# Kernel optimization log

Measured on AMD Instinct MI355X. Metric: run time of the kernel, lower is better.

The kernel has to match this reference:

```python
import jax, jax.numpy as jnp
import numpy as np

HEADS = 4
NBLK = 4
UPS = 4
EPS = 1e-5


def conv3x3(x, w, b):
    # x: NCHW, w: OIHW (3x3, stride 1, pad 1 -> SAME)
    y = jax.lax.conv_general_dilated(x, w, (1, 1), 'SAME',
                                     dimension_numbers=('NCHW', 'OIHW', 'NCHW'))
    return y + b[None, :, None, None]


def layer_norm(x, g, b):
    mu = jnp.mean(x, axis=-1, keepdims=True)
    var = jnp.var(x, axis=-1, keepdims=True)
    return (x - mu) * jax.lax.rsqrt(var + EPS) * g + b


def attention(x, wq, bq, wp, bp):
    # NOTE: the torch module's reshape flattens all windows into one sequence,
    # so this is mathematically global attention over all H*W tokens.
    B, H, W, C = x.shape
    L = H * W
    hd = C // HEADS
    t = x.reshape(B, L, C)
    qkv = (t @ wq + bq).reshape(B, L, 3, HEADS, hd).transpose(2, 0, 3, 1, 4)
    q, k, v = qkv[0], qkv[1], qkv[2]                      # (B, nh, L, hd)
    attn = jax.nn.softmax(jnp.einsum('bnld,bnmd->bnlm', q, k) * (hd ** -0.5), axis=-1)
    o = jnp.einsum('bnlm,bnmd->bnld', attn, v)            # (B, nh, L, hd)
    o = o.transpose(0, 2, 1, 3).reshape(B, L, C)
    return (o @ wp + bp).reshape(B, H, W, C)


def swin_block(x, g1, b1, wq, bq, wp, bp, g2, b2, w1, bf1, w2, bf2):
    shortcut = x
    h = jnp.transpose(x, (0, 2, 3, 1))                    # NHWC
    h = layer_norm(h, g1, b1)
    h = attention(h, wq, bq, wp, bp) + h
    h = layer_norm(h, g2, b2)
    h = (jax.nn.gelu(h @ w1 + bf1, approximate=False) @ w2 + bf2) + h
    return shortcut + jnp.transpose(h, (0, 3, 1, 2))


def pixel_shuffle(x, r):
    B, C, H, W = x.shape
    c = C // (r * r)
    x = x.reshape(B, c, r, r, H, W).transpose(0, 1, 4, 2, 5, 3)
    return x.reshape(B, c, H * r, W * r)


def setup_inputs() -> dict:
    key = jax.random.key(0)
    ks = jax.random.split(key, 16)
    d = 48

    def rn(k, shape, s=0.02):
        return jax.random.normal(k, shape, jnp.float32) * s

    return {
        'x': jax.random.normal(ks[0], (2, 3, 64, 64), jnp.float32),
        'conv_first_w': rn(ks[1], (d, 3, 3, 3)),
        'conv_first_b': jnp.zeros((d,), jnp.float32),
        'norm1_g': jnp.ones((NBLK, d), jnp.float32),
        'norm1_b': jnp.zeros((NBLK, d), jnp.float32),
        'qkv_w': rn(ks[2], (NBLK, d, 3 * d)),
        'qkv_b': jnp.zeros((NBLK, 3 * d), jnp.float32),
        'proj_w': rn(ks[3], (NBLK, d, d)),
        'proj_b': jnp.zeros((NBLK, d), jnp.float32),
        'norm2_g': jnp.ones((NBLK, d), jnp.float32),
        'norm2_b': jnp.zeros((NBLK, d), jnp.float32),
        'fc1_w': rn(ks[4], (NBLK, d, 2 * d)),
        'fc1_b': jnp.zeros((NBLK, 2 * d), jnp.float32),
        'fc2_w': rn(ks[5], (NBLK, 2 * d, d)),
        'fc2_b': jnp.zeros((NBLK, d), jnp.float32),
        'up_w': rn(ks[6], (d * UPS * UPS, d, 3, 3)),
        'up_b': jnp.zeros((d * UPS * UPS,), jnp.float32),
        'last_w': rn(ks[7], (3, d, 3, 3)),
        'last_b': jnp.zeros((3,), jnp.float32),
    }


def reference(x, conv_first_w, conv_first_b, norm1_g, norm1_b, qkv_w, qkv_b,
              proj_w, proj_b, norm2_g, norm2_b, fc1_w, fc1_b, fc2_w, fc2_b,
              up_w, up_b, last_w, last_b):
    h = conv3x3(x, conv_first_w, conv_first_b)
    for i in range(NBLK):
        h = swin_block(h, norm1_g[i], norm1_b[i], qkv_w[i], qkv_b[i],
                       proj_w[i], proj_b[i], norm2_g[i], norm2_b[i],
                       fc1_w[i], fc1_b[i], fc2_w[i], fc2_b[i])
    h = conv3x3(h, up_w, up_b)
    h = pixel_shuffle(h, UPS)
    return conv3x3(h, last_w, last_b)
```

## Files before the change

kernel.cpp:

```cpp
#include <hip/hip_runtime.h>
#include <hip/hip_bf16.h>
#include <math.h>

#define BB 2
#define D 48
#define HH 64
#define WW 64
#define LL 4096
#define NHEADS 4
#define HD 12
#define NBLK 4
#define CUP 768
#define H2 256
#define W2 256

#define NSPLIT 4
#define OPART_STRIDE 393216

typedef __attribute__((ext_vector_type(8))) short short8v;
typedef __attribute__((ext_vector_type(4))) float f32x4;
typedef unsigned long long u64;

__device__ __forceinline__ short f2bf(float f) {
    __hip_bfloat16 h = __float2bfloat16(f);
    union { __hip_bfloat16 b; short s; } u; u.b = h; return u.s;
}
__device__ __forceinline__ float bf2f(short s) {
    union { float f; unsigned u; } x;
    x.u = ((unsigned)(unsigned short)s) << 16;
    return x.f;
}
__device__ __forceinline__ float exp2_raw(float x) {
    float r; asm("v_exp_f32 %0, %1" : "=v"(r) : "v"(x)); return r;
}

__global__ void conv3x3_kernel(const float* __restrict__ in, const float* __restrict__ w,
                               const float* __restrict__ bias, float* __restrict__ out,
                               int Cin, int Cout) {
    int idx = blockIdx.x * blockDim.x + threadIdx.x;
    int total = BB * Cout * HH * WW;
    if (idx >= total) return;
    int x = idx % WW;
    int y = (idx / WW) % HH;
    int co = (idx / (WW * HH)) % Cout;
    int b = idx / (WW * HH * Cout);
    float s = bias[co];
    for (int ci = 0; ci < Cin; ci++) {
        const float* ip = in + ((size_t)(b * Cin + ci) * HH) * WW;
        const float* wp = w + (size_t)(co * Cin + ci) * 9;
        #pragma unroll
        for (int ky = 0; ky < 3; ky++) {
            int iy = y + ky - 1;
            if (iy < 0 || iy >= HH) continue;
            #pragma unroll
            for (int kx = 0; kx < 3; kx++) {
                int ix = x + kx - 1;
                if (ix < 0 || ix >= WW) continue;
                s += ip[iy * WW + ix] * wp[ky * 3 + kx];
            }
        }
    }
    out[idx] = s;
}

__global__ __launch_bounds__(256) void pack_h_kernel(const float* __restrict__ h,
                                                     short* __restrict__ hbfp) {
    int idx = blockIdx.x * 256 + threadIdx.x;
    const int TOT = 2 * 66 * 66 * 48;
    if (idx >= TOT + 64) return;
    if (idx >= TOT) { hbfp[idx] = 0; return; }
    int ci = idx % 48;
    int p = idx / 48;
    int xx = p % 66;
    int q = p / 66;
    int yy = q % 66;
    int b = q / 66;
    short v = 0;
    if (yy >= 1 && yy <= 64 && xx >= 1 && xx <= 64)
        v = f2bf(h[((size_t)(b * 48 + ci) << 12) + (yy - 1) * 64 + (xx - 1)]);
    hbfp[idx] = v;
}

__global__ __launch_bounds__(256) void pack_w_kernel(const float* __restrict__ w,
                                                     short* __restrict__ Wp) {
    int idx = blockIdx.x * 256 + threadIdx.x;
    if (idx >= 48 * 14 * 512) return;
    int j = idx & 7;
    int g = (idx >> 3) & 3;
    int col = (idx >> 5) & 15;
    int s = (idx >> 9) % 14;
    int n16 = idx / (14 * 512);
    int k = 32 * s + 8 * g + j;
    short v = 0;
    if (k < 432) {
        int tap = k / 48, ci = k - tap * 48;
        int co = n16 * 16 + col;
        v = f2bf(w[((size_t)co * 48 + ci) * 9 + tap]);
    }
    Wp[idx] = v;
}

__global__ __launch_bounds__(256) void pack_lw_kernel(const float* __restrict__ w,
                                                      short* __restrict__ Wp2) {
    int idx = blockIdx.x * 256 + threadIdx.x;
    if (idx >= 14 * 512) return;
    int j = idx & 7;
    int g = (idx >> 3) & 3;
    int col = (idx >> 5) & 15;
    int s = idx >> 9;
    int k = 32 * s + 8 * g + j;
    short v = 0;
    if (k < 432 && col < 3) {
        int tap = k / 48, ci = k - tap * 48;
        v = f2bf(w[((size_t)col * 48 + ci) * 9 + tap]);
    }
    Wp2[idx] = v;
}

#define CU_LOADB(P, n) { \
    _Pragma("unroll") \
    for (int s_ = 0; s_ < 14; s_++) \
        P[s_] = *(const short8v*)(Wb + (size_t)(n) * 7168 + s_ * 512); }

#define CU_COMP(P, n) { \
    f32x4 acc = {0.f, 0.f, 0.f, 0.f}; \
    _Pragma("unroll") \
    for (int s_ = 0; s_ < 14; s_++) \
        acc = __builtin_amdgcn_mfma_f32_16x16x32_bf16(av[s_], P[s_], acc, 0, 0, 0); \
    float bval = bias[(n) * 16 + col]; \
    _Pragma("unroll") \
    for (int j = 0; j < 4; j++) \
        Sw[sbase + j * 192 + (n)] = f2bf(acc[j] + bval); }

__global__ __launch_bounds__(128) void conv_up_mfma_kernel(const short* __restrict__ hbfp,
                                                           const short* __restrict__ Wp,
                                                           const float* __restrict__ bias,
                                                           short* __restrict__ U) {
    __shared__ short Sb[2][12288];
    int tid = threadIdx.x;
    int wave = tid >> 6, lane = tid & 63;
    int mt = blockIdx.x * 2 + wave;
    int b = mt >> 8;
    int rem = mt & 255;
    int y = rem >> 2;
    int xt = rem & 3;
    int col = lane & 15;
    int g = lane >> 4;
    int x = xt * 16 + col;

    const short* zb = hbfp + 2 * 66 * 66 * 48;

    short8v av[14];
    #pragma unroll
    for (int s = 0; s < 14; s++) {
        int gg = 4 * s + g;
        int tap = (gg * 171) >> 10;
        int cig = gg - tap * 6;
        int dy = (tap * 11) >> 5;
        int dx = tap - dy * 3;
        const short* ap = hbfp + ((size_t)((b * 66 + y + dy) * 66 + (x + dx)) * 48 + cig * 8);
        ap = (gg < 54) ? ap : zb;
        av[s] = *(const short8v*)ap;
    }

    const short* Wb = Wp + col * 32 + g * 8;
    short* Sw = Sb[wave];
    int dyq = col >> 2, dxq = col & 3;
    int sbase = dyq * 3072 + (16 * g + dxq) * 48;

    short8v Ba[14], Bb[14];
    CU_LOADB(Ba, 0);
    for (int n = 0; n < 48; n += 2) {
        CU_LOADB(Bb, n + 1);
        CU_COMP(Ba, n);
        if (n + 2 < 48) CU_LOADB(Ba, n + 2);
        CU_COMP(Bb, n + 1);
    }

    short* Ub = U + (((size_t)(b * 256 + 4 * y) * 256) + xt * 64) * 48;
    for (int i = lane; i < 1536; i += 64) {
        int row = i / 384;
        int w8 = i - row * 384;
        short8v v = *(const short8v*)(Sw + (size_t)i * 8);
        *(short8v*)(Ub + (size_t)row * 256 * 48 + w8 * 8) = v;
    }
}

__global__ void zero16_kernel(u64* __restrict__ p, int n) {
    int i = blockIdx.x * 256 + threadIdx.x;
    if (i >= n) return;
    u64 fill = 0ull;
    int rel = 8 * i - 2097152;
    if (rel >= 0 && rel < 524288 && (((rel >> 5) & 15) == 12))
        fill = 0x3F803F803F803F80ull;
    p[2 * i] = fill;
    p[2 * i + 1] = fill;
}

__global__ __launch_bounds__(256) void fused_ln1_qkv_kernel(
    const float* __restrict__ hsrc, const float* __restrict__ g1, const float* __restrict__ b1,
    const float* __restrict__ w, const float* __restrict__ bias,
    float* __restrict__ ln1, short* __restrict__ Qbf, short* __restrict__ Kbf,
    short* __restrict__ Vr) {
    __shared__ float hs[48 * 17];
    __shared__ float lnr[16 * 49];
    __shared__ float wl[48 * 144];
    int blk = blockIdx.x;
    int b = blk >> 8;
    int pos0 = (blk & 255) * 16;
    int tid = threadIdx.x;

    for (int i = tid; i < 48 * 144; i += 256) wl[i] = w[i];
    for (int i = tid; i < 48 * 16; i += 256) {
        int ch = i >> 4, p = i & 15;
        hs[ch * 17 + p] = hsrc[((size_t)b * 48 + ch) * 4096 + pos0 + p];
    }
    __syncthreads();

    int tok = tid >> 4, oct = tid & 15;
    int pos = pos0 + tok;
    float v[3];
    float s = 0.f, s2 = 0.f;
    #pragma unroll
    for (int j = 0; j < 3; j++) {
        float x = hs[(oct * 3 + j) * 17 + tok];
        v[j] = x; s += x; s2 += x * x;
    }
    #pragma unroll
    for (int msk = 1; msk < 16; msk <<= 1) {
        s += __shfl_xor(s, msk, 64);
        s2 += __shfl_xor(s2, msk, 64);
    }
    float mu = s * (1.f / 48.f);
    float var = s2 * (1.f / 48.f) - mu * mu;
    float rs = rsqrtf(var + 1e-5f);
    float* go = ln1 + ((size_t)b * 4096 + pos) * 48 + oct * 3;
    #pragma unroll
    for (int j = 0; j < 3; j++) {
        int c = oct * 3 + j;
        float y = (v[j] - mu) * rs * g1[c] + b1[c];
        lnr[tok * 49 + c] = y;
        go[j] = y;
    }
    __syncthreads();

    int c0 = oct * 9;
    float acc[9];
    #pragma unroll
    for (int j = 0; j < 9; j++) acc[j] = bias[c0 + j];
    #pragma unroll 4
    for (int k = 0; k < 48; k++) {
        float a = lnr[tok * 49 + k];
        const float* wr = wl + k * 144 + c0;
        #pragma unroll
        for (int j = 0; j < 9; j++) acc[j] += a * wr[j];
    }

    const float scale = 0.41647023f;
    int sstep = pos >> 5, r = pos & 31;
    int g2 = (r < 16) ? (r >> 2) : ((r - 16) >> 2);
    int j2 = (r < 16) ? (r & 3) : 4 + ((r - 16) & 3);
    #pragma unroll
    for (int j = 0; j < 9; j++) {
        int c = c0 + j;
        int which = (c >= 96) ? 2 : (c >= 48 ? 1 : 0);
        int rem = c - which * 48;
        int hh = rem / 12;
        int dd = rem - hh * 12;
        int bh = b * 4 + hh;
        if (which == 0)
            Qbf[((size_t)bh * 4096 + pos) * 32 + dd] = f2bf(acc[j] * scale);
        else if (which == 1)
            Kbf[((size_t)bh * 4096 + pos) * 32 + dd] = f2bf(acc[j]);
        else
            Vr[((size_t)bh * 128 + sstep) * 512 + dd * 32 + g2 * 8 + j2] = f2bf(acc[j]);
    }
}

__global__ __launch_bounds__(256) void fused_mlp_kernel(
    const float* __restrict__ opart, const float* __restrict__ ssump,
    const float* __restrict__ pwg, const float* __restrict__ pb,
    const float* __restrict__ ln1, const float* __restrict__ g2v, const float* __restrict__ b2v,
    const float* __restrict__ f1w, const float* __restrict__ f1b,
    const float* __restrict__ f2w, const float* __restrict__ f2b,
    float* __restrict__ hbuf) {
    __shared__ float sm[14640];
    float* wp  = sm;
    float* w1  = sm + 2304;
    float* w2  = sm + 6912;
    float* arf = sm + 11520;
    float* lnr = sm + 12304;
    float* m1v = sm + 13088;

    int blk = blockIdx.x;
    int b = blk >> 8;
    int pos0 = (blk & 255) * 16;
    int tid = threadIdx.x;

    for (int i = tid; i < 2304; i += 256) wp[i] = pwg[i];
    for (int i = tid; i < 4608; i += 256) w1[i] = f1w[i];
    for (int i = tid; i < 4608; i += 256) w2[i] = f2w[i];
    for (int i = tid; i < 768; i += 256) {
        int t = i / 48, c = i - (i / 48) * 48;
        int hh = c / 12;
        size_t base = ((size_t)b * 4096 + pos0) * 48 + i;
        float stot = 0.f, s = 0.f;
        #pragma unroll
        for (int sp = 0; sp < NSPLIT; sp++) {
            stot += ssump[((size_t)sp * 8 + b * 4 + hh) * 4096 + pos0 + t];
            s += opart[base + (size_t)sp * OPART_STRIDE];
        }
        arf[t * 49 + c] = s / stot;
    }
    __syncthreads();

    int tok = tid >> 4, oct = tid & 15;
    size_t gtok = (size_t)b * 4096 + pos0 + tok;
    int c0 = oct * 3;
    float acc[3];
    #pragma unroll
    for (int j = 0; j < 3; j++) acc[j] = pb[c0 + j];
    #pragma unroll 4
    for (int k = 0; k < 48; k++) {
        float a = arf[tok * 49 + k];
        const float* wr = wp + k * 48 + c0;
        #pragma unroll
        for (int j = 0; j < 3; j++) acc[j] += a * wr[j];
    }
    const float* rp = ln1 + gtok * 48 + c0;
    float x[3]; float s = 0.f, s2 = 0.f;
    #pragma unroll
    for (int j = 0; j < 3; j++) {
        float t = acc[j] + rp[j];
        x[j] = t; s += t; s2 += t * t;
    }
    #pragma unroll
    for (int msk = 1; msk < 16; msk <<= 1) {
        s += __shfl_xor(s, msk, 64);
        s2 += __shfl_xor(s2, msk, 64);
    }
    float mu = s * (1.f / 48.f), var = s2 * (1.f / 48.f) - mu * mu;
    float rs = rsqrtf(var + 1e-5f);
    #pragma unroll
    for (int j = 0; j < 3; j++) {
        int c = c0 + j;
        lnr[tok * 49 + c] = (x[j] - mu) * rs * g2v[c] + b2v[c];
    }
    __syncthreads();

    int d0 = oct * 6;
    float a2[6];
    #pragma unroll
    for (int j = 0; j < 6; j++) a2[j] = f1b[d0 + j];
    #pragma unroll 4
    for (int k = 0; k < 48; k++) {
        float a = lnr[tok * 49 + k];
        const float* wr = w1 + k * 96 + d0;
        #pragma unroll
        for (int j = 0; j < 6; j++) a2[j] += a * wr[j];
    }
    #pragma unroll
    for (int j = 0; j < 6; j++) {
        float g = a2[j];
        m1v[tok * 97 + d0 + j] = 0.5f * g * (1.f + erff(g * 0.70710678118654752f));
    }
    __syncthreads();

    float f2acc[3];
    #pragma unroll
    for (int j = 0; j < 3; j++) f2acc[j] = f2b[c0 + j];
    #pragma unroll 4
    for (int k = 0; k < 96; k++) {
        float a = m1v[tok * 97 + k];
        const float* wr = w2 + k * 48 + c0;
        #pragma unroll
        for (int j = 0; j < 3; j++) f2acc[j] += a * wr[j];
    }
    __syncthreads();
    #pragma unroll
    for (int j = 0; j < 3; j++)
        arf[tok * 49 + c0 + j] = f2acc[j] + lnr[tok * 49 + c0 + j];
    __syncthreads();

    for (int i = tid; i < 768; i += 256) {
        int c = i >> 4, t = i & 15;
        hbuf[(((size_t)(b * 48 + c)) << 12) + pos0 + t] += arf[t * 49 + c];
    }
}

#define LOADCH(P, c) { \
    _Pragma("unroll") \
    for (int s_ = 0; s_ < 4; s_++) { \
        const short* kp_ = Kb + ((size_t)((c) * 128 + s_ * 32 + col)) * 32 + g * 8; \
        P##k0[s_] = *(const short8v*)(kp_); \
        P##k1[s_] = *(const short8v*)(kp_ + 512); \
        P##v[s_]  = *(const short8v*)(Vrb + ((c) * 4 + s_) * 512 + vbase); \
    } }

#define STEP4(kc0, kc1, vv) { \
    _Pragma("unroll") \
    for (int f_ = 0; f_ < 4; f_++) { \
        f32x4 z_ = {0.f, 0.f, 0.f, 0.f}; \
        f32x4 s1 = __builtin_amdgcn_mfma_f32_16x16x32_bf16(kc0, qb[f_], z_, 0, 0, 0); \
        f32x4 s2 = __builtin_amdgcn_mfma_f32_16x16x32_bf16(kc1, qb[f_], z_, 0, 0, 0); \
        float p0 = exp2_raw(s1[0]), p1 = exp2_raw(s1[1]); \
        float p2 = exp2_raw(s1[2]), p3 = exp2_raw(s1[3]); \
        float p4 = exp2_raw(s2[0]), p5 = exp2_raw(s2[1]); \
        float p6 = exp2_raw(s2[2]), p7 = exp2_raw(s2[3]); \
        union { short8v sv; unsigned u[4]; } pu_; \
        asm("v_cvt_pk_bf16_f32 %0, %1, %2" : "=v"(pu_.u[0]) : "v"(p0), "v"(p1)); \
        asm("v_cvt_pk_bf16_f32 %0, %1, %2" : "=v"(pu_.u[1]) : "v"(p2), "v"(p3)); \
        asm("v_cvt_pk_bf16_f32 %0, %1, %2" : "=v"(pu_.u[2]) : "v"(p4), "v"(p5)); \
        asm("v_cvt_pk_bf16_f32 %0, %1, %2" : "=v"(pu_.u[3]) : "v"(p6), "v"(p7)); \
        o[f_] = __builtin_amdgcn_mfma_f32_16x16x32_bf16(vv, pu_.sv, o[f_], 0, 0, 0); \
    } }

#define COMPUTECH4(P) { \
    STEP4(P##k0[0], P##k1[0], P##v[0]); \
    STEP4(P##k0[1], P##k1[1], P##v[1]); \
    STEP4(P##k0[2], P##k1[2], P##v[2]); \
    STEP4(P##k0[3], P##k1[3], P##v[3]); }

__global__ __launch_bounds__(256) void attn_mfma_kernel(const short* __restrict__ Qbf,
                                                        const short* __restrict__ Kbf,
                                                        const short* __restrict__ Vr,
                                                        float* __restrict__ opart,
                                                        float* __restrict__ ssump) {
    int bid = blockIdx.x;
    int bh = bid & 7;
    int qblk = (bid >> 3) & 15;
    int split = bid >> 7;
    int h = bh & 3, b = bh >> 2;
    int tid = threadIdx.x;
    int wave = tid >> 6;
    int lane = tid & 63;
    int q0 = qblk * 256 + wave * 64;
    int col = lane & 15;
    int g = lane >> 4;

    const short* Kb  = Kbf + (size_t)bh * LL * 32 + (size_t)split * 1024 * 32;
    const short* Vrb = Vr + (size_t)bh * 65536 + (size_t)split * 32 * 512;
    int vbase = col * 32 + g * 8;

    short8v qb[4];
    f32x4 o[4];
    #pragma unroll
    for (int f = 0; f < 4; f++) {
        qb[f] = *(const short8v*)(Qbf + ((size_t)bh * LL + q0 + 16 * f + col) * 32 + g * 8);
        o[f] = (f32x4){0.f, 0.f, 0.f, 0.f};
    }

    short8v a_k0[4], a_k1[4], a_v[4];
    short8v b_k0[4], b_k1[4], b_v[4];

    LOADCH(a_, 0);
    for (int c = 0; c < 8; c += 2) {
        LOADCH(b_, c + 1);
        COMPUTECH4(a_);
        if (c + 2 < 8) LOADCH(a_, c + 2);
        COMPUTECH4(b_);
    }

    #pragma unroll
    for (int f = 0; f < 4; f++) {
        float ss = __shfl(o[f][0], 48 + col, 64);
        float* op = opart + (size_t)split * OPART_STRIDE
                  + ((size_t)b * 4096 + q0 + 16 * f + col) * 48 + h * HD;
        #pragma unroll
        for (int j = 0; j < 4; j++) {
            int d = 4 * g + j;
            if (d < HD)
                op[d] = o[f][j];
        }
        if (lane < 16)
            ssump[((size_t)split * 8 + bh) * 4096 + q0 + 16 * f + col] = ss;
    }
}

__global__ __launch_bounds__(256) void lastconv_mfma_kernel(const short* __restrict__ U,
                                                            const short* __restrict__ Wp2,
                                                            const short* __restrict__ zb,
                                                            const float* __restrict__ bias,
                                                            float* __restrict__ out) {
    int tid = threadIdx.x;
    int wave = tid >> 6, lane = tid & 63;
    int t = blockIdx.x * 4 + wave;
    int xt = t & 15;
    int yy = (t >> 4) & 255;
    int b = t >> 12;
    int col = lane & 15, g = lane >> 4;
    int x = xt * 16 + col;

    const short* Ub = U + (size_t)b * 65536 * 48;
    const short* Bp = Wp2 + col * 32 + g * 8;

    f32x4 acc = {0.f, 0.f, 0.f, 0.f};
    #pragma unroll
    for (int s = 0; s < 14; s++) {
        int gg = 4 * s + g;
        int tap = (gg * 171) >> 10;
        int cig = gg - tap * 6;
        int dy3 = (tap * 11) >> 5;
        int dy = dy3 - 1;
        int dx = tap - dy3 * 3 - 1;
        int yq = yy + dy, xq = x + dx;
        bool ok = (gg < 54) && (yq >= 0) && (yq < 256) && (xq >= 0) && (xq < 256);
        const short* ap = Ub + (ptrdiff_t)(yq * 256 + xq) * 48 + cig * 8;
        ap = ok ? ap : zb;
        short8v av = *(const short8v*)ap;
        short8v bv = *(const short8v*)(Bp + s * 512);
        acc = __builtin_amdgcn_mfma_f32_16x16x32_bf16(av, bv, acc, 0, 0, 0);
    }

    if (col < 3) {
        float bval = bias[col];
        float* op = out + ((size_t)(b * 3 + col) * 256 + yy) * 256 + xt * 16 + 4 * g;
        #pragma unroll
        for (int j = 0; j < 4; j++)
            op[j] = acc[j] + bval;
    }
}

static inline int gs(int n) { return (n + 255) / 256; }

extern "C" void kernel_launch(void* const* d_in, const int* in_sizes, int n_in,
                              void* d_out, int out_size, void* d_ws, size_t ws_size,
                              hipStream_t stream) {
    const float* x    = (const float*)d_in[0];
    const float* cf_w = (const float*)d_in[1];
    const float* cf_b = (const float*)d_in[2];
    const float* n1g  = (const float*)d_in[3];
    const float* n1b  = (const float*)d_in[4];
    const float* qkvw = (const float*)d_in[5];
    const float* qkvb = (const float*)d_in[6];
    const float* pw   = (const float*)d_in[7];
    const float* pb   = (const float*)d_in[8];
    const float* n2g  = (const float*)d_in[9];
    const float* n2b  = (const float*)d_in[10];
    const float* f1w  = (const float*)d_in[11];
    const float* f1b  = (const float*)d_in[12];
    const float* f2w  = (const float*)d_in[13];
    const float* f2b  = (const float*)d_in[14];
    const float* upw  = (const float*)d_in[15];
    const float* upb  = (const float*)d_in[16];
    const float* lw   = (const float*)d_in[17];
    const float* lb   = (const float*)d_in[18];

    float* ws = (float*)d_ws;
    const int S_h = BB * D * LL;
    float* A_h   = ws;
    float* pool  = ws + S_h;
    float* A_ln1 = pool;

    short* U_bf = (short*)pool;
    float* o_part = pool + 1572864;
    short* Qbf  = (short*)(pool + 3538944);
    short* Kbf  = Qbf + BB * NHEADS * LL * 32;
    short* Vr   = Kbf + BB * NHEADS * LL * 32;
    short* hbfp = (short*)(pool + 4849664);
    short* Wp   = (short*)(pool + 5058784);
    short* Wp2  = (short*)(pool + 5230816);
    float* ssum_part = pool + 5898240;

    conv3x3_kernel<<<gs(S_h), 256, 0, stream>>>(x, cf_w, cf_b, A_h, 3, D);

    zero16_kernel<<<1536, 256, 0, stream>>>((u64*)Qbf, 393216);
    pack_w_kernel<<<1344, 256, 0, stream>>>(upw, Wp);
    pack_lw_kernel<<<28, 256, 0, stream>>>(lw, Wp2);

    for (int i = 0; i < NBLK; i++) {
        fused_ln1_qkv_kernel<<<512, 256, 0, stream>>>(
            A_h, n1g + i * D, n1b + i * D,
            qkvw + (size_t)i * D * 3 * D, qkvb + i * 3 * D,
            A_ln1, Qbf, Kbf, Vr);
        attn_mfma_kernel<<<8 * 16 * NSPLIT, 256, 0, stream>>>(Qbf, Kbf, Vr, o_part, ssum_part);
        fused_mlp_kernel<<<512, 256, 0, stream>>>(
            o_part, ssum_part, pw + (size_t)i * D * D, pb + i * D,
            A_ln1, n2g + i * D, n2b + i * D,
            f1w + (size_t)i * D * 2 * D, f1b + i * 2 * D,
            f2w + (size_t)i * 2 * D * D, f2b + i * D,
            A_h);
    }

    pack_h_kernel<<<1634, 256, 0, stream>>>(A_h, hbfp);
    conv_up_mfma_kernel<<<256, 128, 0, stream>>>(hbfp, Wp, upb, U_bf);

    lastconv_mfma_kernel<<<2048, 256, 0, stream>>>(
        U_bf, Wp2, hbfp + 2 * 66 * 66 * 48, lb, (float*)d_out);
}
```

Baseline: 278.9 us.

## Double attention key splits and split conv_up output channels across waves

The attention kernel now splits the key/value sequence into 8 chunks instead of 4, doubling the grid so each block processes half as many key chunks. The partial-output workspace is rearranged so the larger set of partial results fits. The upsampling conv kernel now uses 4 waves per block: two waves share each output tile, each computing half of the 48 output-channel groups, with a block-wide barrier before a cooperative store. This raises parallelism in both kernels, at the cost of more partial sums for the MLP kernel to merge and a synchronisation in conv_up.

Result: no change. 282.7 us (+1.4%).

```diff
diff --git a/kernel.cpp b/kernel.cpp
--- a/kernel.cpp
+++ b/kernel.cpp
@@ -14,7 +14,7 @@
 #define H2 256
 #define W2 256
 
-#define NSPLIT 4
+#define NSPLIT 8
 #define OPART_STRIDE 393216
 
 typedef __attribute__((ext_vector_type(8))) short short8v;
@@ -132,14 +132,16 @@
     for (int j = 0; j < 4; j++) \
         Sw[sbase + j * 192 + (n)] = f2bf(acc[j] + bval); }
 
-__global__ __launch_bounds__(128) void conv_up_mfma_kernel(const short* __restrict__ hbfp,
+__global__ __launch_bounds__(256) void conv_up_mfma_kernel(const short* __restrict__ hbfp,
                                                            const short* __restrict__ Wp,
                                                            const float* __restrict__ bias,
                                                            short* __restrict__ U) {
     __shared__ short Sb[2][12288];
     int tid = threadIdx.x;
     int wave = tid >> 6, lane = tid & 63;
-    int mt = blockIdx.x * 2 + wave;
+    int ss = wave >> 1;
+    int nh = wave & 1;
+    int mt = blockIdx.x * 2 + ss;
     int b = mt >> 8;
     int rem = mt & 255;
     int y = rem >> 2;
@@ -164,24 +166,33 @@
     }
 
     const short* Wb = Wp + col * 32 + g * 8;
-    short* Sw = Sb[wave];
+    short* Sw = Sb[ss];
     int dyq = col >> 2, dxq = col & 3;
     int sbase = dyq * 3072 + (16 * g + dxq) * 48;
 
+    int n0 = nh * 24;
     short8v Ba[14], Bb[14];
-    CU_LOADB(Ba, 0);
-    for (int n = 0; n < 48; n += 2) {
+    CU_LOADB(Ba, n0);
+    for (int n = n0; n < n0 + 24; n += 2) {
         CU_LOADB(Bb, n + 1);
         CU_COMP(Ba, n);
-        if (n + 2 < 48) CU_LOADB(Ba, n + 2);
+        if (n + 2 < n0 + 24) CU_LOADB(Ba, n + 2);
         CU_COMP(Bb, n + 1);
     }
-
-    short* Ub = U + (((size_t)(b * 256 + 4 * y) * 256) + xt * 64) * 48;
-    for (int i = lane; i < 1536; i += 64) {
-        int row = i / 384;
-        int w8 = i - row * 384;
-        short8v v = *(const short8v*)(Sw + (size_t)i * 8);
+    __syncthreads();
+
+    for (int i = tid; i < 3072; i += 256) {
+        int st = i / 1536;
+        int r = i - st * 1536;
+        int row = r / 384;
+        int w8 = r - row * 384;
+        int mts = blockIdx.x * 2 + st;
+        int bs = mts >> 8;
+        int rems = mts & 255;
+        int ys = rems >> 2;
+        int xts = rems & 3;
+        short* Ub = U + (((size_t)(bs * 256 + 4 * ys) * 256) + xts * 64) * 48;
+        short8v v = *(const short8v*)(Sb[st] + (size_t)r * 8);
         *(short8v*)(Ub + (size_t)row * 256 * 48 + w8 * 8) = v;
     }
 }
@@ -438,8 +449,8 @@
     int col = lane & 15;
     int g = lane >> 4;
 
-    const short* Kb  = Kbf + (size_t)bh * LL * 32 + (size_t)split * 1024 * 32;
-    const short* Vrb = Vr + (size_t)bh * 65536 + (size_t)split * 32 * 512;
+    const short* Kb  = Kbf + (size_t)bh * LL * 32 + (size_t)split * 512 * 32;
+    const short* Vrb = Vr + (size_t)bh * 65536 + (size_t)split * 16 * 512;
     int vbase = col * 32 + g * 8;
 
     short8v qb[4];
@@ -454,10 +465,10 @@
     short8v b_k0[4], b_k1[4], b_v[4];
 
     LOADCH(a_, 0);
-    for (int c = 0; c < 8; c += 2) {
+    for (int c = 0; c < 4; c += 2) {
         LOADCH(b_, c + 1);
         COMPUTECH4(a_);
-        if (c + 2 < 8) LOADCH(a_, c + 2);
+        if (c + 2 < 4) LOADCH(a_, c + 2);
         COMPUTECH4(b_);
     }
 
@@ -550,17 +561,17 @@
     const int S_h = BB * D * LL;
     float* A_h   = ws;
     float* pool  = ws + S_h;
-    float* A_ln1 = pool;
-
+
+    float* o_part = pool;
     short* U_bf = (short*)pool;
-    float* o_part = pool + 1572864;
+    float* A_ln1 = pool + 3145728;
     short* Qbf  = (short*)(pool + 3538944);
     short* Kbf  = Qbf + BB * NHEADS * LL * 32;
     short* Vr   = Kbf + BB * NHEADS * LL * 32;
     short* hbfp = (short*)(pool + 4849664);
     short* Wp   = (short*)(pool + 5058784);
     short* Wp2  = (short*)(pool + 5230816);
-    float* ssum_part = pool + 5898240;
+    float* ssum_part = pool + 5234400;
 
     conv3x3_kernel<<<gs(S_h), 256, 0, stream>>>(x, cf_w, cf_b, A_h, 3, D);
 
@@ -583,7 +594,7 @@
     }
 
     pack_h_kernel<<<1634, 256, 0, stream>>>(A_h, hbfp);
-    conv_up_mfma_kernel<<<256, 128, 0, stream>>>(hbfp, Wp, upb, U_bf);
+    conv_up_mfma_kernel<<<256, 256, 0, stream>>>(hbfp, Wp, upb, U_bf);
 
     lastconv_mfma_kernel<<<2048, 256, 0, stream>>>(
         U_bf, Wp2, hbfp + 2 * 66 * 66 * 48, lb, (float*)d_out);
```

## Stage K/V chunks through double-buffered LDS shared by all waves in attention

Applied to the files above, without the earlier changes.

In the attention kernel, the four waves of a block each used to load the same K and V chunks straight from global memory into registers. Now the block loads each chunk cooperatively once, writes it into a double-buffered shared-memory tile, and each wave reads its fragments from there. This cuts redundant global/L2 traffic and register pressure from the old two-set register prefetch. It adds a __syncthreads per chunk, LDS write/read traffic and possible bank conflicts.

New measurement: 284.7 us. +2.0%, slower.

```diff
diff --git a/kernel.cpp b/kernel.cpp
--- a/kernel.cpp
+++ b/kernel.cpp
@@ -388,13 +388,27 @@
     }
 }
 
-#define LOADCH(P, c) { \
+#define STAGE_LOAD(c) { \
+    _Pragma("unroll") \
+    for (int k_ = 0; k_ < 3; k_++) { \
+        int off_ = (tid + k_ * 256) * 8; \
+        stg[k_] = (k_ < 2) \
+            ? *(const short8v*)(Kb + (size_t)(c) * 4096 + off_) \
+            : *(const short8v*)(Vrb + (size_t)(c) * 2048 + (off_ - 4096)); \
+    } }
+
+#define STAGE_WRITE(pb) { \
+    _Pragma("unroll") \
+    for (int k_ = 0; k_ < 3; k_++) \
+        *(short8v*)(kv[pb] + (tid + k_ * 256) * 8) = stg[k_]; }
+
+#define LOADCH_LDS(P, pb) { \
     _Pragma("unroll") \
     for (int s_ = 0; s_ < 4; s_++) { \
-        const short* kp_ = Kb + ((size_t)((c) * 128 + s_ * 32 + col)) * 32 + g * 8; \
+        const short* kp_ = kv[pb] + (s_ * 32 + col) * 32 + g * 8; \
         P##k0[s_] = *(const short8v*)(kp_); \
         P##k1[s_] = *(const short8v*)(kp_ + 512); \
-        P##v[s_]  = *(const short8v*)(Vrb + ((c) * 4 + s_) * 512 + vbase); \
+        P##v[s_]  = *(const short8v*)(kv[pb] + 4096 + s_ * 512 + vbase); \
     } }
 
 #define STEP4(kc0, kc1, vv) { \
@@ -426,6 +440,7 @@
                                                         const short* __restrict__ Vr,
                                                         float* __restrict__ opart,
                                                         float* __restrict__ ssump) {
+    __shared__ short kv[2][6144];
     int bid = blockIdx.x;
     int bh = bid & 7;
     int qblk = (bid >> 3) & 15;
@@ -450,15 +465,18 @@
         o[f] = (f32x4){0.f, 0.f, 0.f, 0.f};
     }
 
+    short8v stg[3];
     short8v a_k0[4], a_k1[4], a_v[4];
-    short8v b_k0[4], b_k1[4], b_v[4];
-
-    LOADCH(a_, 0);
-    for (int c = 0; c < 8; c += 2) {
-        LOADCH(b_, c + 1);
+
+    STAGE_LOAD(0);
+    STAGE_WRITE(0);
+    __syncthreads();
+    for (int c = 0; c < 8; c++) {
+        if (c + 1 < 8) STAGE_LOAD(c + 1);
+        LOADCH_LDS(a_, c & 1);
         COMPUTECH4(a_);
-        if (c + 2 < 8) LOADCH(a_, c + 2);
-        COMPUTECH4(b_);
+        if (c + 1 < 8) STAGE_WRITE((c + 1) & 1);
+        __syncthreads();
     }
 
     #pragma unroll
```
